# Performance work log

Measured on AMD Instinct MI355X. Metric: run time of the kernel, lower is better.

The kernel has to match this reference:

```python
import jax, jax.numpy as jnp
import numpy as np

B, T, C = 2, 2048, 1024
H, GAMMA = 16, 8
D = C // H
SCALE = 1.0 / np.sqrt(D).astype(np.float32)


def setup_inputs() -> dict:
    key = jax.random.key(0)
    ks = jax.random.split(key, 6)
    w = 0.02
    return {
        'x': jax.random.normal(ks[0], (B, T, C), dtype=jnp.float32),
        'Wq': jax.random.normal(ks[1], (C, 2 * C), dtype=jnp.float32) * w,
        'Wk': jax.random.normal(ks[2], (C, 2 * C), dtype=jnp.float32) * w,
        'Wv': jax.random.normal(ks[3], (C, C), dtype=jnp.float32) * w,
        'Wo': jax.random.normal(ks[4], (C, C), dtype=jnp.float32) * w,
        'theta_offset': jax.random.normal(ks[5], (H,), dtype=jnp.float32) * 0.1,
    }


def _heads(t):
    # (B, T, C) -> (B, H, T, D)
    return t.reshape(B, T, H, D).transpose(0, 2, 1, 3)


def reference(x, Wq, Wk, Wv, Wo, theta_offset):
    q_raw = x @ Wq                      # (B, T, 2C)
    k_raw = x @ Wk                      # (B, T, 2C)
    v = _heads(x @ Wv)                  # (B, H, T, D)

    q_amp, q_phase = jnp.split(q_raw, 2, axis=-1)
    k_amp, k_phase = jnp.split(k_raw, 2, axis=-1)
    q_amp = jax.nn.softplus(_heads(q_amp))
    q_phase = _heads(q_phase)
    k_amp = jax.nn.softplus(_heads(k_amp))
    k_phase = _heads(k_phase)

    q_real = q_amp * jnp.cos(q_phase)
    q_imag = q_amp * jnp.sin(q_phase)
    k_real = k_amp * jnp.cos(k_phase)
    k_imag = k_amp * jnp.sin(k_phase)

    scores = (jnp.einsum('bhtd,bhsd->bhts', q_real, k_real)
              + jnp.einsum('bhtd,bhsd->bhts', q_imag, k_imag)) * SCALE

    # theta gating (active since T > GAMMA)
    cycle_ids = jnp.arange(T, dtype=jnp.float32) / GAMMA
    cycle_dist = cycle_ids[None, :] - cycle_ids[:, None]        # (T, T)
    theta_gate = jnp.cos(theta_offset[:, None, None] * cycle_dist)  # (H, T, T)
    scores = scores * theta_gate[None]

    causal = jnp.tril(jnp.ones((T, T), dtype=bool))
    scores = jnp.where(causal[None, None], scores, -jnp.inf)
    attn = jax.nn.softmax(scores, axis=-1)

    out = jnp.einsum('bhts,bhsd->bhtd', attn, v)
    out = out.transpose(0, 2, 1, 3).reshape(B, T, C)
    return out @ Wo
```

## Files before the change

### kernel.cpp

```cpp
#include <hip/hip_runtime.h>
#include <hip/hip_bf16.h>
#include <math.h>

#define Bc 2
#define Tc 2048
#define Cc 1024
#define Hc 16
#define Dc 64

typedef __attribute__((ext_vector_type(8))) short short8;
typedef __attribute__((ext_vector_type(4))) float f32x4;

#define L2E 1.44269504088896f
#define SM_M 20.0f

__device__ __forceinline__ short f2bf(float x) {
    unsigned u = __float_as_uint(x);
    u += 0x7fff + ((u >> 16) & 1);
    return (short)(u >> 16);
}
__device__ __forceinline__ unsigned pack2bf_fast(float a, float b) {
    unsigned ua = __float_as_uint(a) + 0x8000u;
    unsigned ub = __float_as_uint(b) + 0x8000u;
    return __builtin_amdgcn_perm(ub, ua, 0x07060302);
}
__device__ __forceinline__ float softplus_fast(float a) {
    return fmaxf(a, 0.f) + __logf(1.f + __expf(-fabsf(a)));
}

#define RDA(BUF, MH) do {                                                      \
    const short* Ah_ = &Al[BUF][MH][0];                                        \
    _Pragma("unroll") for (int mt_ = 0; mt_ < 4; ++mt_) {                      \
        af[mt_][0] = *(const short8*)&Ah_[(wm*64 + mt_*16 + c)*64 + rsw0];     \
        af[mt_][1] = *(const short8*)&Ah_[(wm*64 + mt_*16 + c)*64 + rsw1];     \
    } } while (0)

#define RDB(BUF, NH) do {                                                      \
    const short* Bh_ = &Bl[BUF][NH][0];                                        \
    _Pragma("unroll") for (int nf_ = 0; nf_ < 2; ++nf_) {                      \
        bfr[NH][nf_][0] = *(const short8*)&Bh_[(wn*32 + nf_*16 + c)*64 + rsw0];\
        bfr[NH][nf_][1] = *(const short8*)&Bh_[(wn*32 + nf_*16 + c)*64 + rsw1];\
    } } while (0)

#define MMQ(MH, NH) do {                                                       \
    _Pragma("unroll") for (int mt_ = 0; mt_ < 4; ++mt_)                        \
    _Pragma("unroll") for (int nf_ = 0; nf_ < 2; ++nf_) {                      \
        acc[MH][NH][mt_][nf_] = __builtin_amdgcn_mfma_f32_16x16x32_bf16(       \
            af[mt_][0], bfr[NH][nf_][0], acc[MH][NH][mt_][nf_], 0, 0, 0);      \
        acc[MH][NH][mt_][nf_] = __builtin_amdgcn_mfma_f32_16x16x32_bf16(       \
            af[mt_][1], bfr[NH][nf_][1], acc[MH][NH][mt_][nf_], 0, 0, 0);      \
    } } while (0)

#define BARw asm volatile("s_barrier" ::: "memory")
#define VMW6 asm volatile("s_waitcnt vmcnt(6)" ::: "memory")
#define VMW0 asm volatile("s_waitcnt vmcnt(0)" ::: "memory")
#define PRIO1 __builtin_amdgcn_s_setprio(1)
#define PRIO0 __builtin_amdgcn_s_setprio(0)

__global__ __launch_bounds__(512, 2) void gemm256_qk(
    const short* __restrict__ A, const short* __restrict__ Bt,
    short* __restrict__ q2, short* __restrict__ k2)
{
    __shared__ __attribute__((aligned(16))) short Al[2][2][128 * 64];
    __shared__ __attribute__((aligned(16))) short Bl[2][2][128 * 64];

    const int tid = threadIdx.x;
    const int wave = tid >> 6, lane = tid & 63;
    const int quad = lane >> 4, c = lane & 15;
    const int wm = wave >> 2, wn = wave & 3;
    const int f = blockIdx.x + 16 * blockIdx.y;
    const int w = (f & 7) * 32 + (f >> 3);
    const int bx = w & 15, by = w >> 4;
    const int m0 = by * 256, n0 = bx * 256;

    const int rsw0 = ((quad * 16) ^ ((c & 7) << 4)) >> 1;
    const int rsw1 = ((64 + quad * 16) ^ ((c & 7) << 4)) >> 1;

    f32x4 acc[2][2][4][2];
#pragma unroll
    for (int a0 = 0; a0 < 2; ++a0)
#pragma unroll
        for (int a1 = 0; a1 < 2; ++a1)
#pragma unroll
            for (int a2 = 0; a2 < 4; ++a2)
#pragma unroll
                for (int a3 = 0; a3 < 2; ++a3)
                    acc[a0][a1][a2][a3] = (f32x4){0.f, 0.f, 0.f, 0.f};

    short8 af[4][2];
    short8 bfr[2][2][2];

    auto stA = [&](int kt, int hh) {
        short* dstb = &Al[kt & 1][hh][0];
#pragma unroll
        for (int j = 0; j < 2; ++j) {
            int ch = j * 512 + tid;
            int row = ch >> 3;
            int os = ((((ch & 7) << 4) ^ ((row & 7) << 4)) >> 1);
            const short* src = A + (size_t)(m0 + hh * 128 + row) * 1024 + kt * 64 + os;
            __builtin_amdgcn_global_load_lds(
                (const __attribute__((address_space(1))) void*)src,
                (__attribute__((address_space(3))) void*)(dstb + (j * 512 + wave * 64) * 8),
                16, 0, 0);
        }
    };
    auto stB = [&](int kt, int hh) {
        short* dstb = &Bl[kt & 1][hh][0];
#pragma unroll
        for (int j = 0; j < 2; ++j) {
            int ch = j * 512 + tid;
            int row = ch >> 3;
            int os = ((((ch & 7) << 4) ^ ((row & 7) << 4)) >> 1);
            const short* src = Bt + (size_t)(n0 + hh * 128 + row) * 1024 + kt * 64 + os;
            __builtin_amdgcn_global_load_lds(
                (const __attribute__((address_space(1))) void*)src,
                (__attribute__((address_space(3))) void*)(dstb + (j * 512 + wave * 64) * 8),
                16, 0, 0);
        }
    };

    stB(0, 0); stA(0, 0); stB(0, 1); stA(0, 1); stB(1, 0); stA(1, 0); stB(1, 1);
    VMW6;
    BARw;

    for (int i = 0; i < 8; ++i) {
        const int e = 2 * i;
        const bool more = (i < 7);
        RDA(0, 0); RDB(0, 0);
        stA(e + 1, 1);
        BARw; PRIO1; MMQ(0, 0); PRIO0; BARw;
        RDB(0, 1);
        if (more) stB(e + 2, 0);
        BARw; PRIO1; MMQ(0, 1); PRIO0; BARw;
        RDA(0, 1);
        if (more) stA(e + 2, 0);
        BARw; PRIO1; MMQ(1, 0); PRIO0; BARw;
        if (more) stB(e + 2, 1);
        BARw; PRIO1; MMQ(1, 1); PRIO0;
        if (more) { VMW6; } else { VMW0; }
        BARw;
        RDA(1, 0); RDB(1, 0);
        if (more) stA(e + 2, 1);
        BARw; PRIO1; MMQ(0, 0); PRIO0; BARw;
        RDB(1, 1);
        if (more) stB(e + 3, 0);
        BARw; PRIO1; MMQ(0, 1); PRIO0; BARw;
        RDA(1, 1);
        if (more) stA(e + 3, 0);
        BARw; PRIO1; MMQ(1, 0); PRIO0; BARw;
        if (more) stB(e + 3, 1);
        BARw; PRIO1; MMQ(1, 1); PRIO0;
        if (more) { VMW6; } else { VMW0; }
        BARw;
    }

    const int d = wn * 16 + c;
#pragma unroll
    for (int mh = 0; mh < 2; ++mh) {
#pragma unroll
        for (int nh = 0; nh < 2; ++nh) {
            const int g = 2 * bx + nh;
            const int isK = g >> 4;
            const int hh = g & 15;
            const float scl = isK ? 1.f : 0.125f;
            short* dst = isK ? k2 : q2;
#pragma unroll
            for (int mt = 0; mt < 4; ++mt) {
#pragma unroll
                for (int reg = 0; reg < 4; ++reg) {
                    int m = m0 + mh * 128 + wm * 64 + mt * 16 + quad * 4 + reg;
                    int bb = m >> 11, tt = m & (Tc - 1);
                    size_t base = (((size_t)bb * Hc + hh) * Tc + tt) * 128;
                    float amp = acc[mh][nh][mt][0][reg];
                    float ph  = acc[mh][nh][mt][1][reg];
                    float sp = softplus_fast(amp) * scl;
                    float sn, cs;
                    __sincosf(ph, &sn, &cs);
                    dst[base + d]      = f2bf(sp * cs);
                    dst[base + d + 64] = f2bf(sp * sn);
                }
            }
        }
    }
}

__global__ __launch_bounds__(256) void gemm_bt64(
    const short* __restrict__ A, const short* __restrict__ Bt,
    float* __restrict__ Cf, int M, int N, int K)
{
    __shared__ __attribute__((aligned(16))) short As[128 * 32];
    __shared__ __attribute__((aligned(16))) short Bs[64 * 32];

    const int tid = threadIdx.x;
    const int lane = tid & 63;
    const int wave = tid >> 6;
    const int quad = lane >> 4, c = lane & 15;
    const int wm = wave >> 1, wn = wave & 1;
    const int m0 = blockIdx.y * 128, n0 = blockIdx.x * 64;

    const int rA0 = tid >> 2,        cA0 = (tid & 3) * 8;
    const int rA1 = (256 + tid) >> 2, cA1 = ((256 + tid) & 3) * 8;
    const int rB = tid >> 2,         cB = (tid & 3) * 8;
    const short* Ag0 = A + (size_t)(m0 + rA0) * K + cA0;
    const short* Ag1 = A + (size_t)(m0 + rA1) * K + cA1;
    const short* Bg = Bt + (size_t)(n0 + rB) * K + cB;
    short* AsW0 = As + tid * 8;
    short* AsW1 = As + (256 + tid) * 8;
    short* BsW = Bs + tid * 8;

    f32x4 acc[4][2];
#pragma unroll
    for (int i = 0; i < 4; ++i)
#pragma unroll
        for (int j = 0; j < 2; ++j)
            acc[i][j] = (f32x4){0.f, 0.f, 0.f, 0.f};

    for (int k0 = 0; k0 < K; k0 += 32) {
        __syncthreads();
        __builtin_amdgcn_global_load_lds(
            (const __attribute__((address_space(1))) void*)(Ag0 + k0),
            (__attribute__((address_space(3))) void*)AsW0, 16, 0, 0);
        __builtin_amdgcn_global_load_lds(
            (const __attribute__((address_space(1))) void*)(Ag1 + k0),
            (__attribute__((address_space(3))) void*)AsW1, 16, 0, 0);
        __builtin_amdgcn_global_load_lds(
            (const __attribute__((address_space(1))) void*)(Bg + k0),
            (__attribute__((address_space(3))) void*)BsW, 16, 0, 0);
        __syncthreads();

        short8 af[4], bf[2];
#pragma unroll
        for (int mt = 0; mt < 4; ++mt)
            af[mt] = *(const short8*)&As[(wm * 64 + mt * 16 + c) * 32 + quad * 8];
#pragma unroll
        for (int nt = 0; nt < 2; ++nt)
            bf[nt] = *(const short8*)&Bs[(wn * 32 + nt * 16 + c) * 32 + quad * 8];
#pragma unroll
        for (int mt = 0; mt < 4; ++mt)
#pragma unroll
            for (int nt = 0; nt < 2; ++nt)
                acc[mt][nt] = __builtin_amdgcn_mfma_f32_16x16x32_bf16(
                    af[mt], bf[nt], acc[mt][nt], 0, 0, 0);
    }

#pragma unroll
    for (int mt = 0; mt < 4; ++mt) {
#pragma unroll
        for (int reg = 0; reg < 4; ++reg) {
            size_t row = m0 + wm * 64 + mt * 16 + quad * 4 + reg;
#pragma unroll
            for (int nt = 0; nt < 2; ++nt) {
                size_t col = n0 + wn * 32 + nt * 16 + c;
                Cf[row * N + col] = acc[mt][nt][reg];
            }
        }
    }
}

__global__ __launch_bounds__(256) void gemm_v2t64(
    const short* __restrict__ A, const short* __restrict__ Bt,
    short* __restrict__ v2t)
{
    __shared__ __attribute__((aligned(16))) short As[128 * 32];
    __shared__ __attribute__((aligned(16))) short Bs[64 * 32];
    __shared__ __attribute__((aligned(16))) short tile[64 * 136];

    const int K = Cc;
    const int tid = threadIdx.x;
    const int lane = tid & 63;
    const int wave = tid >> 6;
    const int quad = lane >> 4, c = lane & 15;
    const int wm = wave >> 1, wn = wave & 1;
    const int m0 = blockIdx.y * 128, n0 = blockIdx.x * 64;

    const int rA0 = tid >> 2,        cA0 = (tid & 3) * 8;
    const int rA1 = (256 + tid) >> 2, cA1 = ((256 + tid) & 3) * 8;
    const int rB = tid >> 2,         cB = (tid & 3) * 8;
    const short* Ag0 = A + (size_t)(m0 + rA0) * K + cA0;
    const short* Ag1 = A + (size_t)(m0 + rA1) * K + cA1;
    const short* Bg = Bt + (size_t)(n0 + rB) * K + cB;
    short* AsW0 = As + tid * 8;
    short* AsW1 = As + (256 + tid) * 8;
    short* BsW = Bs + tid * 8;

    f32x4 acc[4][2];
#pragma unroll
    for (int i = 0; i < 4; ++i)
#pragma unroll
        for (int j = 0; j < 2; ++j)
            acc[i][j] = (f32x4){0.f, 0.f, 0.f, 0.f};

    for (int k0 = 0; k0 < K; k0 += 32) {
        __syncthreads();
        __builtin_amdgcn_global_load_lds(
            (const __attribute__((address_space(1))) void*)(Ag0 + k0),
            (__attribute__((address_space(3))) void*)AsW0, 16, 0, 0);
        __builtin_amdgcn_global_load_lds(
            (const __attribute__((address_space(1))) void*)(Ag1 + k0),
            (__attribute__((address_space(3))) void*)AsW1, 16, 0, 0);
        __builtin_amdgcn_global_load_lds(
            (const __attribute__((address_space(1))) void*)(Bg + k0),
            (__attribute__((address_space(3))) void*)BsW, 16, 0, 0);
        __syncthreads();

        short8 af[4], bf[2];
#pragma unroll
        for (int mt = 0; mt < 4; ++mt)
            af[mt] = *(const short8*)&As[(wm * 64 + mt * 16 + c) * 32 + quad * 8];
#pragma unroll
        for (int nt = 0; nt < 2; ++nt)
            bf[nt] = *(const short8*)&Bs[(wn * 32 + nt * 16 + c) * 32 + quad * 8];
#pragma unroll
        for (int mt = 0; mt < 4; ++mt)
#pragma unroll
            for (int nt = 0; nt < 2; ++nt)
                acc[mt][nt] = __builtin_amdgcn_mfma_f32_16x16x32_bf16(
                    af[mt], bf[nt], acc[mt][nt], 0, 0, 0);
    }

#pragma unroll
    for (int mt = 0; mt < 4; ++mt)
#pragma unroll
        for (int reg = 0; reg < 4; ++reg) {
            int tl = wm * 64 + mt * 16 + quad * 4 + reg;
#pragma unroll
            for (int nt = 0; nt < 2; ++nt)
                tile[(wn * 32 + nt * 16 + c) * 136 + tl] = f2bf(acc[mt][nt][reg]);
        }
    __syncthreads();

    const int b = m0 >> 11, tl0 = m0 & (Tc - 1);
#pragma unroll
    for (int i = 0; i < 4; ++i) {
        int e = i * 256 + tid;
        int n = e >> 4;
        int t8 = (e & 15) * 8;
        int ng = n0 + n, h = ng >> 6, d = ng & 63;
        *(short8*)&v2t[(((size_t)b * Hc + h) * Dc + d) * Tc + tl0 + t8] =
            *(const short8*)&tile[n * 136 + t8];
    }
}

__global__ __launch_bounds__(256) void xconv(const float* __restrict__ x,
                                             short* __restrict__ xb)
{
    int idx = blockIdx.x * 256 + threadIdx.x;
    float4 v = *(const float4*)&x[(size_t)idx * 4];
    short4 o = {f2bf(v.x), f2bf(v.y), f2bf(v.z), f2bf(v.w)};
    short4* dst = (short4*)&xb[(size_t)idx * 4];
    *dst = o;
}

__global__ __launch_bounds__(256) void wtrans_qk(const float* __restrict__ Wq,
                                                 const float* __restrict__ Wk,
                                                 short* __restrict__ Bt)
{
    __shared__ short tile[64][80];
    const int n0 = blockIdx.x * 64, k0 = blockIdx.y * 64;
    const int half = blockIdx.z;
    const float* W = half ? Wk : Wq;
    const int tid = threadIdx.x;
#pragma unroll
    for (int i = 0; i < 4; ++i) {
        int e = i * 256 + tid;
        int k = e >> 4, n4 = (e & 15) * 4;
        float4 v = *(const float4*)&W[(size_t)(k0 + k) * 2048 + n0 + n4];
        tile[k][n4]     = f2bf(v.x);
        tile[k][n4 + 1] = f2bf(v.y);
        tile[k][n4 + 2] = f2bf(v.z);
        tile[k][n4 + 3] = f2bf(v.w);
    }
    __syncthreads();
#pragma unroll
    for (int i = 0; i < 16; ++i) {
        int e = i * 256 + tid;
        int n = e >> 6, k = e & 63;
        int ng = n0 + n;
        int sub = ng >> 10, hh = (ng >> 6) & 15, dd = ng & 63;
        int r = (half * 16 + hh) * 128 + (dd >> 4) * 32 + sub * 16 + (dd & 15);
        Bt[(size_t)r * Cc + k0 + k] = tile[k][n];
    }
}

__global__ __launch_bounds__(256) void wtrans2(const float* __restrict__ Wv,
                                               const float* __restrict__ Wo,
                                               short* __restrict__ WtBase)
{
    __shared__ short tile[64][80];
    const int n0 = blockIdx.x * 64, k0 = blockIdx.y * 64;
    const float* W = blockIdx.z ? Wo : Wv;
    short* Wt = WtBase + (size_t)blockIdx.z * Cc * Cc;
    const int tid = threadIdx.x;
#pragma unroll
    for (int i = 0; i < 4; ++i) {
        int e = i * 256 + tid;
        int k = e >> 4, n4 = (e & 15) * 4;
        float4 v = *(const float4*)&W[(size_t)(k0 + k) * Cc + n0 + n4];
        tile[k][n4]     = f2bf(v.x);
        tile[k][n4 + 1] = f2bf(v.y);
        tile[k][n4 + 2] = f2bf(v.z);
        tile[k][n4 + 3] = f2bf(v.w);
    }
    __syncthreads();
#pragma unroll
    for (int i = 0; i < 16; ++i) {
        int e = i * 256 + tid;
        int n = e >> 6, k = e & 63;
        Wt[(size_t)(n0 + n) * Cc + k0 + k] = tile[k][n];
    }
}

__global__ __launch_bounds__(512, 4) void moire_attn8(
    const short* __restrict__ q2, const short* __restrict__ k2,
    const short* __restrict__ v2t, const float* __restrict__ theta,
    short* __restrict__ att)
{
    __shared__ __attribute__((aligned(16))) short Ks[2][64 * 128];
    __shared__ __attribute__((aligned(16))) short Vt[2][64 * 64];
    __shared__ __attribute__((aligned(16))) short Ps[8][16 * 64];

    const int tid = threadIdx.x;
    const int wave = tid >> 6, lane = tid & 63;
    const int quad = lane >> 4, c = lane & 15;
    const int tx = wave >> 2, gw = wave & 3;
    const int f = blockIdx.x + 16 * (blockIdx.y + 16 * blockIdx.z);
    const int w = (f & 7) * 64 + (f >> 3);
    const int p = w & 15;
    const int hb = w >> 4;
    const int h = hb & 15, b = hb >> 4;
    const int qB = 31 - p;
    const float th = theta[h];

    const short* k2b = k2 + (size_t)(b * Hc + h) * Tc * 128;
    const short* v2b = v2t + (size_t)(b * Hc + h) * Dc * Tc;
    const short* q2b = q2 + (size_t)(b * Hc + h) * Tc * 128;

    int qcur = tx ? qB : p;
    int q0 = qcur * 64;
    const int t_l = gw * 16 + c;

    short8 qf[4];
    {
        const short* qp = q2b + (size_t)(q0 + t_l) * 128;
#pragma unroll
        for (int i = 0; i < 4; ++i)
            qf[i] = *(const short8*)(qp + i * 32 + quad * 8);
    }

    float x0 = th * 0.125f * (float)(q0 + t_l);
    float cb = __cosf(x0), sb = -__sinf(x0);
    float cOff[4][4], sOff[4][4];
#pragma unroll
    for (int mt = 0; mt < 4; ++mt)
#pragma unroll
        for (int reg = 0; reg < 4; ++reg) {
            float a = th * 0.125f * (float)(mt * 16 + quad * 4 + reg);
            cOff[mt][reg] = __cosf(a) * L2E;
            sOff[mt][reg] = __sinf(a) * L2E;
        }
    const float cD = __cosf(8.f * th), sD = __sinf(8.f * th);

    f32x4 oacc[4];
    float lsum = 0.f;
#pragma unroll
    for (int nt = 0; nt < 4; ++nt)
        oacc[nt] = (f32x4){0.f, 0.f, 0.f, 0.f};

    auto stageK_all = [&](int jts, int buf) {
        short* dst = &Ks[buf][0];
        const int s0 = jts * 64;
#pragma unroll
        for (int i = 0; i < 2; ++i) {
            int ch = i * 512 + tid;
            int row = ch >> 4, j = ch & 15;
            const short* src = k2b + (size_t)(s0 + row) * 128 + ((j ^ (row & 15)) << 3);
            __builtin_amdgcn_global_load_lds(
                (const __attribute__((address_space(1))) void*)src,
                (__attribute__((address_space(3))) void*)(dst + (i * 512 + wave * 64) * 8),
                16, 0, 0);
        }
    };
    auto stageV_all = [&](int jts, int buf) {
        short* dst = &Vt[buf][0];
        const int s0 = jts * 64;
        int row = tid >> 3, j = tid & 7;
        const short* src = v2b + (size_t)row * Tc + s0 + ((j ^ (row & 7)) << 3);
        __builtin_amdgcn_global_load_lds(
            (const __attribute__((address_space(1))) void*)src,
            (__attribute__((address_space(3))) void*)(dst + (wave * 64) * 8),
            16, 0, 0);
    };
    auto stage_grp = [&](int jts, int buf) {
        const int s0 = jts * 64;
        const int ltid = tid & 255;
        short* dk = &Ks[buf][0];
#pragma unroll
        for (int jj = 0; jj < 4; ++jj) {
            int ch = jj * 256 + ltid;
            int row = ch >> 4, j = ch & 15;
            const short* src = k2b + (size_t)(s0 + row) * 128 + ((j ^ (row & 15)) << 3);
            __builtin_amdgcn_global_load_lds(
                (const __attribute__((address_space(1))) void*)src,
                (__attribute__((address_space(3))) void*)(dk + (jj * 256 + gw * 64) * 8),
                16, 0, 0);
        }
        short* dv = &Vt[buf][0];
#pragma unroll
        for (int jj = 0; jj < 2; ++jj) {
            int ch = jj * 256 + ltid;
            int row = ch >> 3, j = ch & 7;
            const short* src = v2b + (size_t)row * Tc + s0 + ((j ^ (row & 7)) << 3);
            __builtin_amdgcn_global_load_lds(
                (const __attribute__((address_space(1))) void*)src,
                (__attribute__((address_space(3))) void*)(dv + (jj * 256 + gw * 64) * 8),
                16, 0, 0);
        }
    };

    auto do_s = [&](int jt, int buf) {
        const short* KsB = &Ks[buf][0];
        const bool diag = (jt == qcur);

        f32x4 s_acc[4];
#pragma unroll
        for (int mt = 0; mt < 4; ++mt) {
            f32x4 a = {0.f, 0.f, 0.f, 0.f};
#pragma unroll
            for (int kk = 0; kk < 4; ++kk) {
                short8 kf = *(const short8*)&KsB[(mt * 16 + c) * 128 +
                                                 (((kk * 4 + quad) ^ c) << 3)];
                a = __builtin_amdgcn_mfma_f32_16x16x32_bf16(kf, qf[kk], a, 0, 0, 0);
            }
            s_acc[mt] = a;
        }

#pragma unroll
        for (int mt = 0; mt < 4; ++mt) {
            float pv[4];
#pragma unroll
            for (int reg = 0; reg < 4; ++reg) {
                float g2 = cb * cOff[mt][reg] - sb * sOff[mt][reg];
                float arg = fmaf(s_acc[mt][reg], g2, -SM_M * L2E);
                if (diag && (mt * 16 + quad * 4 + reg) > t_l) arg = -1e30f;
                pv[reg] = exp2f(arg);
            }
            lsum += (pv[0] + pv[1]) + (pv[2] + pv[3]);
            uint2 pk = {pack2bf_fast(pv[0], pv[1]), pack2bf_fast(pv[2], pv[3])};
            int slot = ((mt * 2 + (quad >> 1)) ^ (c & 7));
            *(uint2*)&Ps[wave][c * 64 + slot * 8 + (quad & 1) * 4] = pk;
        }

        float ncb = cb * cD - sb * sD;
        sb = sb * cD + cb * sD;
        cb = ncb;
    };

    auto do_pv = [&](int buf) {
        const short* VtB = &Vt[buf][0];
        short8 pf[2];
#pragma unroll
        for (int kk = 0; kk < 2; ++kk)
            pf[kk] = *(const short8*)&Ps[wave][c * 64 +
                         (((kk * 4 + quad) ^ (c & 7)) << 3)];
#pragma unroll
        for (int nt = 0; nt < 4; ++nt)
#pragma unroll
            for (int kk = 0; kk < 2; ++kk) {
                short8 vf = *(const short8*)&VtB[(nt * 16 + c) * 64 +
                             (((kk * 4 + quad) ^ (c & 7)) << 3)];
                oacc[nt] = __builtin_amdgcn_mfma_f32_16x16x32_bf16(
                    pf[kk], vf, oacc[nt], 0, 0, 0);
            }
    };

    auto write_out = [&]() {
        float l = lsum;
        l += __shfl_xor(l, 16);
        l += __shfl_xor(l, 32);
        float il = 1.f / l;
        float ilr[4];
#pragma unroll
        for (int reg = 0; reg < 4; ++reg)
            ilr[reg] = __shfl(il, quad * 4 + reg);
#pragma unroll
        for (int reg = 0; reg < 4; ++reg) {
            int t_o = q0 + gw * 16 + quad * 4 + reg;
#pragma unroll
            for (int nt = 0; nt < 4; ++nt)
                att[(size_t)(b * Tc + t_o) * Cc + h * Dc + nt * 16 + c] =
                    f2bf(oacc[nt][reg] * ilr[reg]);
        }
    };

    stageK_all(0, 0); stageV_all(0, 0);
    for (int jt = 0; jt <= p; ++jt) {
        __syncthreads();
        stageK_all(jt + 1, (jt + 1) & 1);
        stageV_all(jt + 1, (jt + 1) & 1);
        do_s(jt, jt & 1);
        do_pv(jt & 1);
    }
    const int slotB = (p + 1) & 1, slotA = slotB ^ 1;

    __syncthreads();
    if (tx == 0) {
        write_out();
#pragma unroll
        for (int nt = 0; nt < 4; ++nt)
            oacc[nt] = (f32x4){0.f, 0.f, 0.f, 0.f};
        lsum = 0.f;
        qcur = qB; q0 = qB * 64;
        const short* qp = q2b + (size_t)(q0 + t_l) * 128;
#pragma unroll
        for (int i = 0; i < 4; ++i)
            qf[i] = *(const short8*)(qp + i * 32 + quad * 8);
        float a = th * 0.125f * (1088.f - (float)(q0 + t_l));
        __sincosf(a, &sb, &cb);
    } else {
        do_s(p + 1, slotB);
        do_pv(slotB);
    }

    for (int i = 0; i <= 14 - p; ++i) {
        const int jt = tx ? (p + 2 + i) : (17 + i);
        const int sl = tx ? slotB : slotA;
        __syncthreads();
        stage_grp(jt, sl);
        __syncthreads();
        do_s(jt, sl);
        do_pv(sl);
    }

    __syncthreads();
    float* Cmb = (float*)&Ks[0][0];
    if (tx == 0) {
        float* pp = Cmb + (size_t)(gw * 64 + lane) * 20;
#pragma unroll
        for (int nt = 0; nt < 4; ++nt) *(f32x4*)(pp + nt * 4) = oacc[nt];
        pp[16] = lsum;
    }
    __syncthreads();
    if (tx == 1) {
        const float* pp = Cmb + (size_t)(gw * 64 + lane) * 20;
#pragma unroll
        for (int nt = 0; nt < 4; ++nt)
            oacc[nt] += *(const f32x4*)(pp + nt * 4);
        lsum += pp[16];
        write_out();
    }
}

extern "C" void kernel_launch(void* const* d_in, const int* in_sizes, int n_in,
                              void* d_out, int out_size, void* d_ws, size_t ws_size,
                              hipStream_t stream)
{
    const float* x     = (const float*)d_in[0];
    const float* Wq    = (const float*)d_in[1];
    const float* Wk    = (const float*)d_in[2];
    const float* Wv    = (const float*)d_in[3];
    const float* Wo    = (const float*)d_in[4];
    const float* theta = (const float*)d_in[5];
    float* out = (float*)d_out;

    const int M = Bc * Tc;
    char* ws = (char*)d_ws;
    const size_t MB = 1 << 20;
    short* xb   = (short*)(ws);
    short* Bqk  = (short*)(ws + 8 * MB);
    short* Wvt  = (short*)(ws + 16 * MB);
    short* Wot  = (short*)(ws + 18 * MB);
    short* v2t  = (short*)(ws + 28 * MB);
    short* attb = (short*)(ws + 36 * MB);
    short* q2   = (short*)(ws + 44 * MB);
    short* k2   = (short*)d_out;

    xconv<<<(size_t)M * Cc / 1024, 256, 0, stream>>>(x, xb);
    wtrans_qk<<<dim3(2048 / 64, Cc / 64, 2), 256, 0, stream>>>(Wq, Wk, Bqk);
    wtrans2<<<dim3(Cc / 64, Cc / 64, 2), 256, 0, stream>>>(Wv, Wo, Wvt);

    gemm256_qk<<<dim3(4096 / 256, M / 256), 512, 0, stream>>>(xb, Bqk, q2, k2);
    gemm_v2t64<<<dim3(Cc / 64, M / 128), 256, 0, stream>>>(xb, Wvt, v2t);

    moire_attn8<<<dim3(16, Hc, Bc), 512, 0, stream>>>(q2, k2, v2t, theta, attb);

    gemm_bt64<<<dim3(Cc / 64, M / 128), 256, 0, stream>>>(
        attb, Wot, out, M, Cc, Cc);
}
```

Before: 227.2 us.

## Load K and V fragments directly from global memory, dropping LDS staging

```diff
diff --git a/kernel.cpp b/kernel.cpp
--- a/kernel.cpp
+++ b/kernel.cpp
@@ -410,14 +410,13 @@
     }
 }
 
-__global__ __launch_bounds__(512, 4) void moire_attn8(
+__global__ __launch_bounds__(512, 4) void moire_attn11(
     const short* __restrict__ q2, const short* __restrict__ k2,
     const short* __restrict__ v2t, const float* __restrict__ theta,
     short* __restrict__ att)
 {
-    __shared__ __attribute__((aligned(16))) short Ks[2][64 * 128];
-    __shared__ __attribute__((aligned(16))) short Vt[2][64 * 64];
     __shared__ __attribute__((aligned(16))) short Ps[8][16 * 64];
+    __shared__ __attribute__((aligned(16))) float Cmb[256 * 20];
 
     const int tid = threadIdx.x;
     const int wave = tid >> 6, lane = tid & 63;
@@ -466,59 +465,11 @@
     for (int nt = 0; nt < 4; ++nt)
         oacc[nt] = (f32x4){0.f, 0.f, 0.f, 0.f};
 
-    auto stageK_all = [&](int jts, int buf) {
-        short* dst = &Ks[buf][0];
-        const int s0 = jts * 64;
-#pragma unroll
-        for (int i = 0; i < 2; ++i) {
-            int ch = i * 512 + tid;
-            int row = ch >> 4, j = ch & 15;
-            const short* src = k2b + (size_t)(s0 + row) * 128 + ((j ^ (row & 15)) << 3);
-            __builtin_amdgcn_global_load_lds(
-                (const __attribute__((address_space(1))) void*)src,
-                (__attribute__((address_space(3))) void*)(dst + (i * 512 + wave * 64) * 8),
-                16, 0, 0);
-        }
-    };
-    auto stageV_all = [&](int jts, int buf) {
-        short* dst = &Vt[buf][0];
-        const int s0 = jts * 64;
-        int row = tid >> 3, j = tid & 7;
-        const short* src = v2b + (size_t)row * Tc + s0 + ((j ^ (row & 7)) << 3);
-        __builtin_amdgcn_global_load_lds(
-            (const __attribute__((address_space(1))) void*)src,
-            (__attribute__((address_space(3))) void*)(dst + (wave * 64) * 8),
-            16, 0, 0);
-    };
-    auto stage_grp = [&](int jts, int buf) {
-        const int s0 = jts * 64;
-        const int ltid = tid & 255;
-        short* dk = &Ks[buf][0];
-#pragma unroll
-        for (int jj = 0; jj < 4; ++jj) {
-            int ch = jj * 256 + ltid;
-            int row = ch >> 4, j = ch & 15;
-            const short* src = k2b + (size_t)(s0 + row) * 128 + ((j ^ (row & 15)) << 3);
-            __builtin_amdgcn_global_load_lds(
-                (const __attribute__((address_space(1))) void*)src,
-                (__attribute__((address_space(3))) void*)(dk + (jj * 256 + gw * 64) * 8),
-                16, 0, 0);
-        }
-        short* dv = &Vt[buf][0];
-#pragma unroll
-        for (int jj = 0; jj < 2; ++jj) {
-            int ch = jj * 256 + ltid;
-            int row = ch >> 3, j = ch & 7;
-            const short* src = v2b + (size_t)row * Tc + s0 + ((j ^ (row & 7)) << 3);
-            __builtin_amdgcn_global_load_lds(
-                (const __attribute__((address_space(1))) void*)src,
-                (__attribute__((address_space(3))) void*)(dv + (jj * 256 + gw * 64) * 8),
-                16, 0, 0);
-        }
-    };
-
-    auto do_s = [&](int jt, int buf) {
-        const short* KsB = &Ks[buf][0];
+    const short* kRow = k2b + (size_t)c * 128 + quad * 8;
+    const short* vRow = v2b + (size_t)c * Tc + quad * 8;
+
+    auto do_s = [&](int jt) {
+        const short* Kt = kRow + (size_t)jt * 8192;
         const bool diag = (jt == qcur);
 
         f32x4 s_acc[4];
@@ -527,8 +478,7 @@
             f32x4 a = {0.f, 0.f, 0.f, 0.f};
 #pragma unroll
             for (int kk = 0; kk < 4; ++kk) {
-                short8 kf = *(const short8*)&KsB[(mt * 16 + c) * 128 +
-                                                 (((kk * 4 + quad) ^ c) << 3)];
+                short8 kf = *(const short8*)(Kt + mt * 2048 + kk * 32);
                 a = __builtin_amdgcn_mfma_f32_16x16x32_bf16(kf, qf[kk], a, 0, 0, 0);
             }
             s_acc[mt] = a;
@@ -555,8 +505,8 @@
         cb = ncb;
     };
 
-    auto do_pv = [&](int buf) {
-        const short* VtB = &Vt[buf][0];
+    auto do_pv = [&](int jt) {
+        const short* Vt = vRow + jt * 64;
         short8 pf[2];
 #pragma unroll
         for (int kk = 0; kk < 2; ++kk)
@@ -566,8 +516,7 @@
         for (int nt = 0; nt < 4; ++nt)
 #pragma unroll
             for (int kk = 0; kk < 2; ++kk) {
-                short8 vf = *(const short8*)&VtB[(nt * 16 + c) * 64 +
-                             (((kk * 4 + quad) ^ (c & 7)) << 3)];
+                short8 vf = *(const short8*)(Vt + (size_t)nt * 16 * Tc + kk * 32);
                 oacc[nt] = __builtin_amdgcn_mfma_f32_16x16x32_bf16(
                     pf[kk], vf, oacc[nt], 0, 0, 0);
             }
@@ -592,18 +541,8 @@
         }
     };
 
-    stageK_all(0, 0); stageV_all(0, 0);
-    for (int jt = 0; jt <= p; ++jt) {
-        __syncthreads();
-        stageK_all(jt + 1, (jt + 1) & 1);
-        stageV_all(jt + 1, (jt + 1) & 1);
-        do_s(jt, jt & 1);
-        do_pv(jt & 1);
-    }
-    const int slotB = (p + 1) & 1, slotA = slotB ^ 1;
-
-    __syncthreads();
     if (tx == 0) {
+        for (int jt = 0; jt <= p; ++jt) { do_s(jt); do_pv(jt); }
         write_out();
 #pragma unroll
         for (int nt = 0; nt < 4; ++nt)
@@ -616,23 +555,12 @@
             qf[i] = *(const short8*)(qp + i * 32 + quad * 8);
         float a = th * 0.125f * (1088.f - (float)(q0 + t_l));
         __sincosf(a, &sb, &cb);
+        for (int jt = 17; jt <= qB; ++jt) { do_s(jt); do_pv(jt); }
     } else {
-        do_s(p + 1, slotB);
-        do_pv(slotB);
-    }
-
-    for (int i = 0; i <= 14 - p; ++i) {
-        const int jt = tx ? (p + 2 + i) : (17 + i);
-        const int sl = tx ? slotB : slotA;
-        __syncthreads();
-        stage_grp(jt, sl);
-        __syncthreads();
-        do_s(jt, sl);
-        do_pv(sl);
+        for (int jt = 0; jt <= 16; ++jt) { do_s(jt); do_pv(jt); }
     }
 
     __syncthreads();
-    float* Cmb = (float*)&Ks[0][0];
     if (tx == 0) {
         float* pp = Cmb + (size_t)(gw * 64 + lane) * 20;
 #pragma unroll
@@ -681,7 +609,7 @@
     gemm256_qk<<<dim3(4096 / 256, M / 256), 512, 0, stream>>>(xb, Bqk, q2, k2);
     gemm_v2t64<<<dim3(Cc / 64, M / 128), 256, 0, stream>>>(xb, Wvt, v2t);
 
-    moire_attn8<<<dim3(16, Hc, Bc), 512, 0, stream>>>(q2, k2, v2t, theta, attb);
+    moire_attn11<<<dim3(16, Hc, Bc), 512, 0, stream>>>(q2, k2, v2t, theta, attb);
 
     gemm_bt64<<<dim3(Cc / 64, M / 128), 256, 0, stream>>>(
         attb, Wot, out, M, Cc, Cc);
```

New measurement: 352.4 us. +55.1%, slower.

## Fuse V projection into the 256-tile QK GEMM with transposed LDS epilogue

Applied to the files above, without the earlier changes.

```diff
diff --git a/kernel.cpp b/kernel.cpp
--- a/kernel.cpp
+++ b/kernel.cpp
@@ -57,9 +57,9 @@
 #define PRIO1 __builtin_amdgcn_s_setprio(1)
 #define PRIO0 __builtin_amdgcn_s_setprio(0)
 
-__global__ __launch_bounds__(512, 2) void gemm256_qk(
+__global__ __launch_bounds__(512, 2) void gemm256_qkv(
     const short* __restrict__ A, const short* __restrict__ Bt,
-    short* __restrict__ q2, short* __restrict__ k2)
+    short* __restrict__ q2, short* __restrict__ k2, short* __restrict__ v2t)
 {
     __shared__ __attribute__((aligned(16))) short Al[2][2][128 * 64];
     __shared__ __attribute__((aligned(16))) short Bl[2][2][128 * 64];
@@ -68,9 +68,9 @@
     const int wave = tid >> 6, lane = tid & 63;
     const int quad = lane >> 4, c = lane & 15;
     const int wm = wave >> 2, wn = wave & 3;
-    const int f = blockIdx.x + 16 * blockIdx.y;
-    const int w = (f & 7) * 32 + (f >> 3);
-    const int bx = w & 15, by = w >> 4;
+    const int f = blockIdx.x + 20 * blockIdx.y;
+    const int w = (f & 7) * 40 + (f >> 3);
+    const int bx = w % 20, by = w / 20;
     const int m0 = by * 256, n0 = bx * 256;
 
     const int rsw0 = ((quad * 16) ^ ((c & 7) << 4)) >> 1;
@@ -154,32 +154,69 @@
         BARw;
     }
 
-    const int d = wn * 16 + c;
-#pragma unroll
-    for (int mh = 0; mh < 2; ++mh) {
-#pragma unroll
-        for (int nh = 0; nh < 2; ++nh) {
-            const int g = 2 * bx + nh;
-            const int isK = g >> 4;
-            const int hh = g & 15;
-            const float scl = isK ? 1.f : 0.125f;
-            short* dst = isK ? k2 : q2;
-#pragma unroll
-            for (int mt = 0; mt < 4; ++mt) {
-#pragma unroll
-                for (int reg = 0; reg < 4; ++reg) {
-                    int m = m0 + mh * 128 + wm * 64 + mt * 16 + quad * 4 + reg;
-                    int bb = m >> 11, tt = m & (Tc - 1);
-                    size_t base = (((size_t)bb * Hc + hh) * Tc + tt) * 128;
-                    float amp = acc[mh][nh][mt][0][reg];
-                    float ph  = acc[mh][nh][mt][1][reg];
-                    float sp = softplus_fast(amp) * scl;
-                    float sn, cs;
-                    __sincosf(ph, &sn, &cs);
-                    dst[base + d]      = f2bf(sp * cs);
-                    dst[base + d + 64] = f2bf(sp * sn);
+    if (bx < 16) {
+        const int d = wn * 16 + c;
+#pragma unroll
+        for (int mh = 0; mh < 2; ++mh) {
+#pragma unroll
+            for (int nh = 0; nh < 2; ++nh) {
+                const int g = 2 * bx + nh;
+                const int isK = g >> 4;
+                const int hh = g & 15;
+                const float scl = isK ? 1.f : 0.125f;
+                short* dst = isK ? k2 : q2;
+#pragma unroll
+                for (int mt = 0; mt < 4; ++mt) {
+#pragma unroll
+                    for (int reg = 0; reg < 4; ++reg) {
+                        int m = m0 + mh * 128 + wm * 64 + mt * 16 + quad * 4 + reg;
+                        int bb = m >> 11, tt = m & (Tc - 1);
+                        size_t base = (((size_t)bb * Hc + hh) * Tc + tt) * 128;
+                        float amp = acc[mh][nh][mt][0][reg];
+                        float ph  = acc[mh][nh][mt][1][reg];
+                        float sp = softplus_fast(amp) * scl;
+                        float sn, cs;
+                        __sincosf(ph, &sn, &cs);
+                        dst[base + d]      = f2bf(sp * cs);
+                        dst[base + d + 64] = f2bf(sp * sn);
+                    }
                 }
             }
+        }
+    } else {
+        short* vt_lds = &Al[0][0][0];
+        const int nv0 = (bx - 16) * 256;
+        const int bb = m0 >> 11, tt0 = m0 & (Tc - 1);
+#pragma unroll
+        for (int tc = 0; tc < 4; ++tc) {
+            if (wm == (tc & 1)) {
+                const int mh = tc >> 1;
+#pragma unroll
+                for (int nh = 0; nh < 2; ++nh)
+#pragma unroll
+                    for (int nf = 0; nf < 2; ++nf) {
+                        int nn = nh * 128 + wn * 32 + nf * 16 + c;
+#pragma unroll
+                        for (int mt = 0; mt < 4; ++mt)
+#pragma unroll
+                            for (int reg = 0; reg < 4; ++reg) {
+                                int tl = mt * 16 + quad * 4 + reg;
+                                vt_lds[nn * 80 + tl] =
+                                    f2bf(acc[mh][nh][mt][nf][reg]);
+                            }
+                    }
+            }
+            __syncthreads();
+#pragma unroll
+            for (int i2 = 0; i2 < 4; ++i2) {
+                int e = i2 * 512 + tid;
+                int nn = e >> 3, t8 = (e & 7) * 8;
+                int ng = nv0 + nn, hh = ng >> 6, dd = ng & 63;
+                *(short8*)&v2t[(((size_t)bb * Hc + hh) * Dc + dd) * Tc +
+                               tt0 + tc * 64 + t8] =
+                    *(const short8*)&vt_lds[nn * 80 + t8];
+            }
+            __syncthreads();
         }
     }
 }
@@ -257,90 +294,6 @@
     }
 }
 
-__global__ __launch_bounds__(256) void gemm_v2t64(
-    const short* __restrict__ A, const short* __restrict__ Bt,
-    short* __restrict__ v2t)
-{
-    __shared__ __attribute__((aligned(16))) short As[128 * 32];
-    __shared__ __attribute__((aligned(16))) short Bs[64 * 32];
-    __shared__ __attribute__((aligned(16))) short tile[64 * 136];
-
-    const int K = Cc;
-    const int tid = threadIdx.x;
-    const int lane = tid & 63;
-    const int wave = tid >> 6;
-    const int quad = lane >> 4, c = lane & 15;
-    const int wm = wave >> 1, wn = wave & 1;
-    const int m0 = blockIdx.y * 128, n0 = blockIdx.x * 64;
-
-    const int rA0 = tid >> 2,        cA0 = (tid & 3) * 8;
-    const int rA1 = (256 + tid) >> 2, cA1 = ((256 + tid) & 3) * 8;
-    const int rB = tid >> 2,         cB = (tid & 3) * 8;
-    const short* Ag0 = A + (size_t)(m0 + rA0) * K + cA0;
-    const short* Ag1 = A + (size_t)(m0 + rA1) * K + cA1;
-    const short* Bg = Bt + (size_t)(n0 + rB) * K + cB;
-    short* AsW0 = As + tid * 8;
-    short* AsW1 = As + (256 + tid) * 8;
-    short* BsW = Bs + tid * 8;
-
-    f32x4 acc[4][2];
-#pragma unroll
-    for (int i = 0; i < 4; ++i)
-#pragma unroll
-        for (int j = 0; j < 2; ++j)
-            acc[i][j] = (f32x4){0.f, 0.f, 0.f, 0.f};
-
-    for (int k0 = 0; k0 < K; k0 += 32) {
-        __syncthreads();
-        __builtin_amdgcn_global_load_lds(
-            (const __attribute__((address_space(1))) void*)(Ag0 + k0),
-            (__attribute__((address_space(3))) void*)AsW0, 16, 0, 0);
-        __builtin_amdgcn_global_load_lds(
-            (const __attribute__((address_space(1))) void*)(Ag1 + k0),
-            (__attribute__((address_space(3))) void*)AsW1, 16, 0, 0);
-        __builtin_amdgcn_global_load_lds(
-            (const __attribute__((address_space(1))) void*)(Bg + k0),
-            (__attribute__((address_space(3))) void*)BsW, 16, 0, 0);
-        __syncthreads();
-
-        short8 af[4], bf[2];
-#pragma unroll
-        for (int mt = 0; mt < 4; ++mt)
-            af[mt] = *(const short8*)&As[(wm * 64 + mt * 16 + c) * 32 + quad * 8];
-#pragma unroll
-        for (int nt = 0; nt < 2; ++nt)
-            bf[nt] = *(const short8*)&Bs[(wn * 32 + nt * 16 + c) * 32 + quad * 8];
-#pragma unroll
-        for (int mt = 0; mt < 4; ++mt)
-#pragma unroll
-            for (int nt = 0; nt < 2; ++nt)
-                acc[mt][nt] = __builtin_amdgcn_mfma_f32_16x16x32_bf16(
-                    af[mt], bf[nt], acc[mt][nt], 0, 0, 0);
-    }
-
-#pragma unroll
-    for (int mt = 0; mt < 4; ++mt)
-#pragma unroll
-        for (int reg = 0; reg < 4; ++reg) {
-            int tl = wm * 64 + mt * 16 + quad * 4 + reg;
-#pragma unroll
-            for (int nt = 0; nt < 2; ++nt)
-                tile[(wn * 32 + nt * 16 + c) * 136 + tl] = f2bf(acc[mt][nt][reg]);
-        }
-    __syncthreads();
-
-    const int b = m0 >> 11, tl0 = m0 & (Tc - 1);
-#pragma unroll
-    for (int i = 0; i < 4; ++i) {
-        int e = i * 256 + tid;
-        int n = e >> 4;
-        int t8 = (e & 15) * 8;
-        int ng = n0 + n, h = ng >> 6, d = ng & 63;
-        *(short8*)&v2t[(((size_t)b * Hc + h) * Dc + d) * Tc + tl0 + t8] =
-            *(const short8*)&tile[n * 136 + t8];
-    }
-}
-
 __global__ __launch_bounds__(256) void xconv(const float* __restrict__ x,
                                              short* __restrict__ xb)
 {
@@ -666,8 +619,7 @@
     char* ws = (char*)d_ws;
     const size_t MB = 1 << 20;
     short* xb   = (short*)(ws);
-    short* Bqk  = (short*)(ws + 8 * MB);
-    short* Wvt  = (short*)(ws + 16 * MB);
+    short* Bqkv = (short*)(ws + 8 * MB);
     short* Wot  = (short*)(ws + 18 * MB);
     short* v2t  = (short*)(ws + 28 * MB);
     short* attb = (short*)(ws + 36 * MB);
@@ -675,11 +627,12 @@
     short* k2   = (short*)d_out;
 
     xconv<<<(size_t)M * Cc / 1024, 256, 0, stream>>>(x, xb);
-    wtrans_qk<<<dim3(2048 / 64, Cc / 64, 2), 256, 0, stream>>>(Wq, Wk, Bqk);
-    wtrans2<<<dim3(Cc / 64, Cc / 64, 2), 256, 0, stream>>>(Wv, Wo, Wvt);
-
-    gemm256_qk<<<dim3(4096 / 256, M / 256), 512, 0, stream>>>(xb, Bqk, q2, k2);
-    gemm_v2t64<<<dim3(Cc / 64, M / 128), 256, 0, stream>>>(xb, Wvt, v2t);
+    wtrans_qk<<<dim3(2048 / 64, Cc / 64, 2), 256, 0, stream>>>(Wq, Wk, Bqkv);
+    wtrans2<<<dim3(Cc / 64, Cc / 64, 2), 256, 0, stream>>>(
+        Wv, Wo, Bqkv + (size_t)4096 * Cc);
+
+    gemm256_qkv<<<dim3(5120 / 256, M / 256), 512, 0, stream>>>(
+        xb, Bqkv, q2, k2, v2t);
 
     moire_attn8<<<dim3(16, Hc, Bc), 512, 0, stream>>>(q2, k2, v2t, theta, attb);
 
```

New measurement: 241.2 us. +6.2%, slower.
